# Performance work log

Measured on AMD Instinct MI355X. Metric: run time of the kernel, lower is better.

The kernel has to match this reference:

```python
import jax, jax.numpy as jnp
import numpy as np

B, T, C = 4, 4096, 1024
HS = 64


def setup_inputs() -> dict:
    key = jax.random.key(0)
    k0, k1, k2, k3 = jax.random.split(key, 4)
    std = 1.0 / np.sqrt(C)
    return {
        "x": jax.random.normal(k0, (B, T, C), dtype=jnp.float32),
        "Wk": jax.random.normal(k1, (HS, C), dtype=jnp.float32) * std,
        "Wq": jax.random.normal(k2, (HS, C), dtype=jnp.float32) * std,
        "Wv": jax.random.normal(k3, (HS, C), dtype=jnp.float32) * std,
        "i": 0,
        "embed_dim": 1024,
        "head_size_sel": 64,
    }


def reference(x, Wk, Wq, Wv, i, embed_dim, head_size_sel):
    # NAS slicing of inputs/weights (static ints -> jit-safe)
    xs = x[:, :, :embed_dim]                      # [B,T,E]
    kw = Wk[:head_size_sel, :embed_dim]           # [H,E]
    qw = Wq[:head_size_sel, :embed_dim]
    vw = Wv[:head_size_sel, :embed_dim]
    k = jnp.einsum('bte,he->bth', xs, kw)         # [B,T,H]
    q = jnp.einsum('bte,he->bth', xs, qw)
    v = jnp.einsum('bte,he->bth', xs, vw)
    scale = jnp.asarray(head_size_sel, x.dtype) ** -0.5
    wei = jnp.einsum('bqh,bkh->bqk', q, k) * scale  # [B,T,T] full score matrix
    Tlen = x.shape[1]
    causal = jnp.tril(jnp.ones((Tlen, Tlen), dtype=bool))
    wei = jnp.where(causal[None, :, :], wei, -jnp.inf)
    wei = jax.nn.softmax(wei, axis=-1)
    # dropout: eval mode (identity) for deterministic reference
    out = jnp.einsum('bqk,bkh->bqh', wei, v)      # [B,T,H]
    return out
```

## Files before the change

kernel.cpp:

```cpp
#include <hip/hip_runtime.h>
#include <math.h>

typedef __bf16 bf16_t;
typedef __bf16 bf16x8 __attribute__((ext_vector_type(8)));
typedef __bf16 bf16x4 __attribute__((ext_vector_type(4)));
typedef float  floatx4 __attribute__((ext_vector_type(4)));

#define TT   4096
#define CD   1024
#define HSZ  64
#define NROW 16384
#define NEG_BIG (-1e30f)

#define WB_OFF 0
#define Q_OFF  196608
#define K_OFF  (196608 + NROW * HSZ)
#define V_OFF  (196608 + 2 * NROW * HSZ)

#if __has_builtin(__builtin_amdgcn_exp2f)
__device__ __forceinline__ float fexp2(float x) { return __builtin_amdgcn_exp2f(x); }
#else
__device__ __forceinline__ float fexp2(float x) { return exp2f(x); }
#endif

__device__ __forceinline__ float qmax(float v) {
  v = fmaxf(v, __shfl_xor(v, 16));
  v = fmaxf(v, __shfl_xor(v, 32));
  return v;
}
__device__ __forceinline__ float qsum(float v) {
  v += __shfl_xor(v, 16);
  v += __shfl_xor(v, 32);
  return v;
}

__global__ __launch_bounds__(256, 1) void wcvt_kernel(
    const float* __restrict__ Wk, const float* __restrict__ Wq,
    const float* __restrict__ Wv, bf16_t* __restrict__ Wb)
{
  const int t    = blockIdx.x * 256 + threadIdx.x;
  const int e    = t * 4;
  const int tile = e >> 9;
  const int kc   = tile / 12;
  const int t12  = tile - kc * 12;
  const int r    = e & 511;
  const int lane = r >> 3;
  const int j0   = r & 7;
  const int wsel = t12 >> 2;
  const int nt   = t12 & 3;
  const int n    = nt * 16 + (lane & 15);
  const int k    = kc * 32 + (lane >> 4) * 8 + j0;
  const float* src = (wsel == 0) ? Wq : (wsel == 1) ? Wk : Wv;
  float4 f = *(const float4*)(src + n * CD + k);
  bf16x4 o;
  o[0] = (bf16_t)f.x; o[1] = (bf16_t)f.y; o[2] = (bf16_t)f.z; o[3] = (bf16_t)f.w;
  *(bf16x4*)(Wb + e) = o;
}

__global__ __launch_bounds__(512, 4) void qkv_proj_kernel(
    const float* __restrict__ x, const bf16_t* __restrict__ Wb,
    bf16_t* __restrict__ qg, bf16_t* __restrict__ kfr, bf16_t* __restrict__ vfr)
{
  __shared__ __align__(16) floatx4 red[3][2][12][64];

  const int tid  = threadIdx.x;
  const int lane = tid & 63;
  const int wave = tid >> 6;
  const int kh   = wave >> 1;
  const int mt   = wave & 1;
  const int mr   = lane & 15;
  const int quad = lane >> 4;
  const int m0   = blockIdx.x * 32 + mt * 16;

  floatx4 acc[12];
#pragma unroll
  for (int i = 0; i < 12; ++i) acc[i] = (floatx4){0.f, 0.f, 0.f, 0.f};

  const float* xp = x + (size_t)(m0 + mr) * CD + quad * 8;

  for (int kc = kh * 8; kc < kh * 8 + 8; ++kc) {
    float4 xa = *(const float4*)(xp + kc * 32);
    float4 xb = *(const float4*)(xp + kc * 32 + 4);
    const bf16_t* wp = Wb + kc * 6144 + lane * 8;
    bf16x8 af;
    af[0]=(bf16_t)xa.x; af[1]=(bf16_t)xa.y; af[2]=(bf16_t)xa.z; af[3]=(bf16_t)xa.w;
    af[4]=(bf16_t)xb.x; af[5]=(bf16_t)xb.y; af[6]=(bf16_t)xb.z; af[7]=(bf16_t)xb.w;
#pragma unroll
    for (int i = 0; i < 12; ++i) {
      bf16x8 wf = *(const bf16x8*)(wp + i * 512);
      acc[i] = __builtin_amdgcn_mfma_f32_16x16x32_bf16(af, wf, acc[i], 0, 0, 0);
    }
  }

  if (kh != 0) {
#pragma unroll
    for (int i = 0; i < 12; ++i)
      red[kh - 1][mt][i][lane] = acc[i];
  }
  __syncthreads();
  if (kh == 0) {
    const float qscale = 0.18033688011112042f;
#pragma unroll
    for (int i = 0; i < 12; ++i) {
      floatx4 a = acc[i];
      a += red[0][mt][i][lane];
      a += red[1][mt][i][lane];
      a += red[2][mt][i][lane];
      const int wsel = i >> 2;
      const int nt   = i & 3;
#pragma unroll
      for (int r = 0; r < 4; ++r) {
        const int trow = m0 + quad * 4 + r;
        const int h    = nt * 16 + mr;
        const float v  = a[r];
        if (wsel == 0) {
          qg[(size_t)trow * HSZ + h] = (bf16_t)(v * qscale);
        } else if (wsel == 1) {
          const size_t adr = ((((size_t)(trow >> 6)) * 4 + ((trow >> 4) & 3)) * 2
                              + (h >> 5)) * 512
                             + ((h >> 3) & 3) * 128 + (trow & 15) * 8 + (h & 7);
          kfr[adr] = (bf16_t)v;
        } else {
          const size_t adr = ((((size_t)(trow >> 6)) * 2 + ((trow >> 5) & 1)) * 4
                              + (h >> 4)) * 512
                             + ((trow >> 3) & 3) * 128 + (h & 15) * 8 + (trow & 7);
          vfr[adr] = (bf16_t)v;
        }
      }
    }
  }
}

__device__ __forceinline__ void softmax_step(
    floatx4 (&sv)[4], float& mstv, float& lstv, floatx4 (&ov)[4],
    bf16_t* plp, const int mr, const int quad)
{
  float a = fmaxf(fmaxf(sv[0][0], sv[0][1]), fmaxf(sv[0][2], sv[0][3]));
  float b = fmaxf(fmaxf(sv[1][0], sv[1][1]), fmaxf(sv[1][2], sv[1][3]));
  float c = fmaxf(fmaxf(sv[2][0], sv[2][1]), fmaxf(sv[2][2], sv[2][3]));
  float d = fmaxf(fmaxf(sv[3][0], sv[3][1]), fmaxf(sv[3][2], sv[3][3]));
  float mx = fmaxf(fmaxf(a, b), fmaxf(c, d));
  mx = qmax(mx);
  const float mnew = fmaxf(mstv, mx);
  float rs = 0.f;
#pragma unroll
  for (int nt = 0; nt < 4; ++nt) {
    const float p0 = fexp2(sv[nt][0] - mnew);
    const float p1 = fexp2(sv[nt][1] - mnew);
    const float p2 = fexp2(sv[nt][2] - mnew);
    const float p3 = fexp2(sv[nt][3] - mnew);
    rs += (p0 + p1) + (p2 + p3);
    bf16x4 w;
    w[0] = (bf16_t)p0; w[1] = (bf16_t)p1; w[2] = (bf16_t)p2; w[3] = (bf16_t)p3;
    *(bf16x4*)(plp + mr * 72 + nt * 16 + quad * 4) = w;
  }
  if (__all(mx <= mstv)) {
    lstv += rs;
  } else {
    const float alpha = fexp2(mstv - mnew);
    mstv = mnew;
    lstv = alpha * lstv + rs;
#pragma unroll
    for (int nt = 0; nt < 4; ++nt)
#pragma unroll
      for (int r = 0; r < 4; ++r) ov[nt][r] *= alpha;
  }
}

__global__ __launch_bounds__(1024, 4) void attn_kernel(
    const bf16_t* __restrict__ qg, const bf16_t* __restrict__ kfr,
    const bf16_t* __restrict__ vfr, float* __restrict__ out)
{
  __shared__ __align__(16) char smem[73728];
  __shared__ float cml[16][16][2];
  bf16_t* plds = (bf16_t*)smem;
  float (*cmbo)[16][68] = (float (*)[16][68])smem;

  const int tid  = threadIdx.x;
  const int lane = tid & 63;
  const int wave = tid >> 6;
  const int mr   = lane & 15;
  const int quad = lane >> 4;

  const int bid = blockIdx.x;
  const int b   = bid & 3;
  const int pr  = bid >> 2;
  const int gA  = pr;
  const int gB  = 127 - pr;
  const int nAw = (gA >> 1) + 1;
  const int nBw = (gB >> 1) + 1;
  int na = (16 * nAw + ((nAw + nBw) >> 1)) / (nAw + nBw);
  na = na < 1 ? 1 : (na > 15 ? 15 : na);

  const bool inA   = wave < na;
  const int g      = inA ? gA : gB;
  const int slot   = inA ? wave : wave - na;
  const int nsplit = inA ? na : 16 - na;
  const int q0     = g * 32;
  const int ktmax  = g >> 1;

  const size_t baseq = (size_t)b * TT * HSZ;
  const bf16_t* kb = kfr + (size_t)b * 64 * 4096;
  const bf16_t* vb = vfr + (size_t)b * 64 * 4096;

  bf16_t* pl0 = plds + wave * 2304;
  bf16_t* pl1 = pl0 + 1152;

  bf16x8 qf[2][2];
#pragma unroll
  for (int s = 0; s < 2; ++s) {
    const bf16_t* qp = qg + baseq + (size_t)(q0 + s * 16 + mr) * HSZ + quad * 8;
    qf[s][0] = *(const bf16x8*)qp;
    qf[s][1] = *(const bf16x8*)(qp + 32);
  }

  floatx4 o0[4], o1[4];
#pragma unroll
  for (int i = 0; i < 4; ++i) {
    o0[i] = (floatx4){0.f, 0.f, 0.f, 0.f};
    o1[i] = (floatx4){0.f, 0.f, 0.f, 0.f};
  }
  float mst[2] = {NEG_BIG, NEG_BIG};
  float lst[2] = {0.f, 0.f};

  for (int kt = slot; kt <= ktmax; kt += nsplit) {
    const int k0 = kt * 64;

    floatx4 s0[4], s1[4];
#pragma unroll
    for (int i = 0; i < 4; ++i) {
      s0[i] = (floatx4){0.f, 0.f, 0.f, 0.f};
      s1[i] = (floatx4){0.f, 0.f, 0.f, 0.f};
    }
#pragma unroll
    for (int nt = 0; nt < 4; ++nt) {
      const bf16_t* kp = kb + ((size_t)kt * 4 + nt) * 1024 + lane * 8;
      bf16x8 kb0 = *(const bf16x8*)kp;
      bf16x8 kb1 = *(const bf16x8*)(kp + 512);
      s0[nt] = __builtin_amdgcn_mfma_f32_16x16x32_bf16(kb0, qf[0][0], s0[nt], 0, 0, 0);
      s0[nt] = __builtin_amdgcn_mfma_f32_16x16x32_bf16(kb1, qf[0][1], s0[nt], 0, 0, 0);
      s1[nt] = __builtin_amdgcn_mfma_f32_16x16x32_bf16(kb0, qf[1][0], s1[nt], 0, 0, 0);
      s1[nt] = __builtin_amdgcn_mfma_f32_16x16x32_bf16(kb1, qf[1][1], s1[nt], 0, 0, 0);
    }

    if (kt == ktmax) {
      const int qa0 = q0 + mr;
#pragma unroll
      for (int nt = 0; nt < 4; ++nt) {
#pragma unroll
        for (int r = 0; r < 4; ++r) {
          const int kv = k0 + nt * 16 + quad * 4 + r;
          if (kv > qa0)      s0[nt][r] = NEG_BIG;
          if (kv > qa0 + 16) s1[nt][r] = NEG_BIG;
        }
      }
    }

    softmax_step(s0, mst[0], lst[0], o0, pl0, mr, quad);

    bf16x8 vfa[4];
#pragma unroll
    for (int nt = 0; nt < 4; ++nt)
      vfa[nt] = *(const bf16x8*)(vb + ((size_t)kt * 8 + nt) * 512 + lane * 8);

    softmax_step(s1, mst[1], lst[1], o1, pl1, mr, quad);

    bf16x8 vfb[4];
#pragma unroll
    for (int nt = 0; nt < 4; ++nt)
      vfb[nt] = *(const bf16x8*)(vb + ((size_t)kt * 8 + nt) * 512 + 2048 + lane * 8);

    {
      bf16x8 pa0 = *(bf16x8*)&pl0[mr * 72 + quad * 8];
      bf16x8 pa1 = *(bf16x8*)&pl1[mr * 72 + quad * 8];
#pragma unroll
      for (int nt = 0; nt < 4; ++nt) {
        o0[nt] = __builtin_amdgcn_mfma_f32_16x16x32_bf16(vfa[nt], pa0, o0[nt], 0, 0, 0);
        o1[nt] = __builtin_amdgcn_mfma_f32_16x16x32_bf16(vfa[nt], pa1, o1[nt], 0, 0, 0);
      }
      bf16x8 pb0 = *(bf16x8*)&pl0[mr * 72 + 32 + quad * 8];
      bf16x8 pb1 = *(bf16x8*)&pl1[mr * 72 + 32 + quad * 8];
#pragma unroll
      for (int nt = 0; nt < 4; ++nt) {
        o0[nt] = __builtin_amdgcn_mfma_f32_16x16x32_bf16(vfb[nt], pb0, o0[nt], 0, 0, 0);
        o1[nt] = __builtin_amdgcn_mfma_f32_16x16x32_bf16(vfb[nt], pb1, o1[nt], 0, 0, 0);
      }
    }
  }

  __syncthreads();
#pragma unroll
  for (int s = 0; s < 2; ++s) {
    const float lsum = qsum(lst[s]);
    if (lane < 16) {
      cml[wave][lane][0] = mst[s];
      cml[wave][lane][1] = lsum;
    }
    __syncthreads();
    {
      const int lo = inA ? 0 : na;
      const int hi = inA ? na : 16;
      float mstar = cml[lo][mr][0];
      for (int i = lo + 1; i < hi; ++i) mstar = fmaxf(mstar, cml[i][mr][0]);
      const float scale = fexp2(mst[s] - mstar);
#pragma unroll
      for (int nt = 0; nt < 4; ++nt) {
        floatx4 t;
#pragma unroll
        for (int r = 0; r < 4; ++r) t[r] = (s ? o1[nt][r] : o0[nt][r]) * scale;
        *(floatx4*)&cmbo[wave][mr][nt * 16 + quad * 4] = t;
      }
    }
    __syncthreads();
    {
      const int grp = tid >> 9;
      const int row = (tid >> 5) & 15;
      const int c0  = (tid & 31) * 2;
      const int lo  = grp ? na : 0;
      const int hi  = grp ? 16 : na;
      const int gq0 = (grp ? gB : gA) * 32 + s * 16;
      float mstar = cml[lo][row][0];
      for (int i = lo + 1; i < hi; ++i) mstar = fmaxf(mstar, cml[i][row][0]);
      float l = 0.f;
      for (int i = lo; i < hi; ++i)
        l += cml[i][row][1] * fexp2(cml[i][row][0] - mstar);
      float sx = 0.f, sy = 0.f;
      for (int i = lo; i < hi; ++i) {
        float2 v = *(float2*)&cmbo[i][row][c0];
        sx += v.x; sy += v.y;
      }
      const float invl = 1.0f / l;
      float2 res; res.x = sx * invl; res.y = sy * invl;
      *(float2*)(out + baseq + (size_t)(gq0 + row) * HSZ + c0) = res;
    }
    __syncthreads();
  }
}

extern "C" void kernel_launch(void* const* d_in, const int* in_sizes, int n_in,
                              void* d_out, int out_size, void* d_ws, size_t ws_size,
                              hipStream_t stream) {
  const float* x  = (const float*)d_in[0];
  const float* Wk = (const float*)d_in[1];
  const float* Wq = (const float*)d_in[2];
  const float* Wv = (const float*)d_in[3];
  float* out = (float*)d_out;

  bf16_t* ws  = (bf16_t*)d_ws;
  bf16_t* Wb  = ws + WB_OFF;
  bf16_t* qg  = ws + Q_OFF;
  bf16_t* kfr = ws + K_OFF;
  bf16_t* vfr = ws + V_OFF;

  wcvt_kernel<<<dim3(192), dim3(256), 0, stream>>>(Wk, Wq, Wv, Wb);
  qkv_proj_kernel<<<dim3(512), dim3(512), 0, stream>>>(x, Wb, qg, kfr, vfr);
  attn_kernel<<<dim3(256), dim3(1024), 0, stream>>>(qg, kfr, vfr, out);
}
```

Before: 149.9 us.

## Retile QKV projection to 64 rows per block with split N across waves

The QKV projection block now covers 64 rows instead of 32, with each wave handling 4 M-tiles and 6 of the 12 N-tiles rather than 1 M-tile and 12 N-tiles. Each weight fragment is reused across four row tiles, which cuts weight loads per MFMA, and the grid is halved to 256 blocks. In exchange each wave reads four times as much x, the cross-K reduction becomes a two-phase pass with extra barriers to fit shared memory, register pressure rises (launch bounds lowered to 2), and fewer blocks run on a large GPU.

Result: slower. 155.4 us (+3.7%).

```diff
diff --git a/kernel.cpp b/kernel.cpp
--- a/kernel.cpp
+++ b/kernel.cpp
@@ -57,74 +57,121 @@
   *(bf16x4*)(Wb + e) = o;
 }
 
-__global__ __launch_bounds__(512, 4) void qkv_proj_kernel(
+__global__ __launch_bounds__(512, 2) void qkv_proj_kernel(
     const float* __restrict__ x, const bf16_t* __restrict__ Wb,
     bf16_t* __restrict__ qg, bf16_t* __restrict__ kfr, bf16_t* __restrict__ vfr)
 {
-  __shared__ __align__(16) floatx4 red[3][2][12][64];
+  __shared__ __align__(16) floatx4 red[3][24][64];
 
   const int tid  = threadIdx.x;
   const int lane = tid & 63;
   const int wave = tid >> 6;
   const int kh   = wave >> 1;
-  const int mt   = wave & 1;
+  const int ng   = wave & 1;
   const int mr   = lane & 15;
   const int quad = lane >> 4;
-  const int m0   = blockIdx.x * 32 + mt * 16;
-
-  floatx4 acc[12];
-#pragma unroll
-  for (int i = 0; i < 12; ++i) acc[i] = (floatx4){0.f, 0.f, 0.f, 0.f};
+  const int m0   = blockIdx.x * 64;
+
+  floatx4 acc[4][6];
+#pragma unroll
+  for (int mt = 0; mt < 4; ++mt)
+#pragma unroll
+    for (int i = 0; i < 6; ++i) acc[mt][i] = (floatx4){0.f, 0.f, 0.f, 0.f};
 
   const float* xp = x + (size_t)(m0 + mr) * CD + quad * 8;
+  const bf16_t* wbase = Wb + ng * 3072 + lane * 8;
 
   for (int kc = kh * 8; kc < kh * 8 + 8; ++kc) {
-    float4 xa = *(const float4*)(xp + kc * 32);
-    float4 xb = *(const float4*)(xp + kc * 32 + 4);
-    const bf16_t* wp = Wb + kc * 6144 + lane * 8;
-    bf16x8 af;
-    af[0]=(bf16_t)xa.x; af[1]=(bf16_t)xa.y; af[2]=(bf16_t)xa.z; af[3]=(bf16_t)xa.w;
-    af[4]=(bf16_t)xb.x; af[5]=(bf16_t)xb.y; af[6]=(bf16_t)xb.z; af[7]=(bf16_t)xb.w;
-#pragma unroll
-    for (int i = 0; i < 12; ++i) {
-      bf16x8 wf = *(const bf16x8*)(wp + i * 512);
-      acc[i] = __builtin_amdgcn_mfma_f32_16x16x32_bf16(af, wf, acc[i], 0, 0, 0);
-    }
-  }
-
-  if (kh != 0) {
-#pragma unroll
-    for (int i = 0; i < 12; ++i)
-      red[kh - 1][mt][i][lane] = acc[i];
+    float4 xa[4], xb[4];
+#pragma unroll
+    for (int mt = 0; mt < 4; ++mt) {
+      xa[mt] = *(const float4*)(xp + (size_t)mt * 16 * CD + kc * 32);
+      xb[mt] = *(const float4*)(xp + (size_t)mt * 16 * CD + kc * 32 + 4);
+    }
+    const bf16_t* wp = wbase + kc * 6144;
+    bf16x8 wf[6];
+#pragma unroll
+    for (int i = 0; i < 6; ++i) wf[i] = *(const bf16x8*)(wp + i * 512);
+    bf16x8 af[4];
+#pragma unroll
+    for (int mt = 0; mt < 4; ++mt) {
+      af[mt][0]=(bf16_t)xa[mt].x; af[mt][1]=(bf16_t)xa[mt].y;
+      af[mt][2]=(bf16_t)xa[mt].z; af[mt][3]=(bf16_t)xa[mt].w;
+      af[mt][4]=(bf16_t)xb[mt].x; af[mt][5]=(bf16_t)xb[mt].y;
+      af[mt][6]=(bf16_t)xb[mt].z; af[mt][7]=(bf16_t)xb[mt].w;
+    }
+#pragma unroll
+    for (int i = 0; i < 6; ++i)
+#pragma unroll
+      for (int mt = 0; mt < 4; ++mt)
+        acc[mt][i] = __builtin_amdgcn_mfma_f32_16x16x32_bf16(af[mt], wf[i], acc[mt][i], 0, 0, 0);
+  }
+
+  if (ng == 0 && kh != 0) {
+#pragma unroll
+    for (int mt = 0; mt < 4; ++mt)
+#pragma unroll
+      for (int i = 0; i < 6; ++i)
+        red[kh - 1][mt * 6 + i][lane] = acc[mt][i];
   }
   __syncthreads();
+  if (ng == 0 && kh == 0) {
+#pragma unroll
+    for (int mt = 0; mt < 4; ++mt)
+#pragma unroll
+      for (int i = 0; i < 6; ++i) {
+        acc[mt][i] += red[0][mt * 6 + i][lane];
+        acc[mt][i] += red[1][mt * 6 + i][lane];
+        acc[mt][i] += red[2][mt * 6 + i][lane];
+      }
+  }
+  __syncthreads();
+  if (ng == 1 && kh != 0) {
+#pragma unroll
+    for (int mt = 0; mt < 4; ++mt)
+#pragma unroll
+      for (int i = 0; i < 6; ++i)
+        red[kh - 1][mt * 6 + i][lane] = acc[mt][i];
+  }
+  __syncthreads();
+  if (ng == 1 && kh == 0) {
+#pragma unroll
+    for (int mt = 0; mt < 4; ++mt)
+#pragma unroll
+      for (int i = 0; i < 6; ++i) {
+        acc[mt][i] += red[0][mt * 6 + i][lane];
+        acc[mt][i] += red[1][mt * 6 + i][lane];
+        acc[mt][i] += red[2][mt * 6 + i][lane];
+      }
+  }
+
   if (kh == 0) {
     const float qscale = 0.18033688011112042f;
 #pragma unroll
-    for (int i = 0; i < 12; ++i) {
-      floatx4 a = acc[i];
-      a += red[0][mt][i][lane];
-      a += red[1][mt][i][lane];
-      a += red[2][mt][i][lane];
-      const int wsel = i >> 2;
-      const int nt   = i & 3;
-#pragma unroll
-      for (int r = 0; r < 4; ++r) {
-        const int trow = m0 + quad * 4 + r;
-        const int h    = nt * 16 + mr;
-        const float v  = a[r];
-        if (wsel == 0) {
-          qg[(size_t)trow * HSZ + h] = (bf16_t)(v * qscale);
-        } else if (wsel == 1) {
-          const size_t adr = ((((size_t)(trow >> 6)) * 4 + ((trow >> 4) & 3)) * 2
-                              + (h >> 5)) * 512
-                             + ((h >> 3) & 3) * 128 + (trow & 15) * 8 + (h & 7);
-          kfr[adr] = (bf16_t)v;
-        } else {
-          const size_t adr = ((((size_t)(trow >> 6)) * 2 + ((trow >> 5) & 1)) * 4
-                              + (h >> 4)) * 512
-                             + ((trow >> 3) & 3) * 128 + (h & 15) * 8 + (trow & 7);
-          vfr[adr] = (bf16_t)v;
+    for (int mt = 0; mt < 4; ++mt) {
+#pragma unroll
+      for (int i = 0; i < 6; ++i) {
+        const int t12  = ng * 6 + i;
+        const int wsel = t12 >> 2;
+        const int nt   = t12 & 3;
+#pragma unroll
+        for (int r = 0; r < 4; ++r) {
+          const int trow = m0 + mt * 16 + quad * 4 + r;
+          const int h    = nt * 16 + mr;
+          const float v  = acc[mt][i][r];
+          if (wsel == 0) {
+            qg[(size_t)trow * HSZ + h] = (bf16_t)(v * qscale);
+          } else if (wsel == 1) {
+            const size_t adr = ((((size_t)(trow >> 6)) * 4 + ((trow >> 4) & 3)) * 2
+                                + (h >> 5)) * 512
+                               + ((h >> 3) & 3) * 128 + (trow & 15) * 8 + (h & 7);
+            kfr[adr] = (bf16_t)v;
+          } else {
+            const size_t adr = ((((size_t)(trow >> 6)) * 2 + ((trow >> 5) & 1)) * 4
+                                + (h >> 4)) * 512
+                               + ((trow >> 3) & 3) * 128 + (h & 15) * 8 + (trow & 7);
+            vfr[adr] = (bf16_t)v;
+          }
         }
       }
     }
@@ -353,6 +400,6 @@
   bf16_t* vfr = ws + V_OFF;
 
   wcvt_kernel<<<dim3(192), dim3(256), 0, stream>>>(Wk, Wq, Wv, Wb);
-  qkv_proj_kernel<<<dim3(512), dim3(512), 0, stream>>>(x, Wb, qg, kfr, vfr);
+  qkv_proj_kernel<<<dim3(256), dim3(512), 0, stream>>>(x, Wb, qg, kfr, vfr);
   attn_kernel<<<dim3(256), dim3(1024), 0, stream>>>(qg, kfr, vfr, out);
 }
```
